# Optimization experiments

Hardware: AMD Instinct MI355X
Metric: run time of the kernel (lower is better)

Reference implementation:

```python
import jax, jax.numpy as jnp
import numpy as np

# ---- static structure for the 28x28 image grid ----
H = 28
V = H * H          # 784 vertices
T = 25             # landscape sample points
K_MAX = 2          # landscape orders kept
M0 = 0.05          # DTM mass parameter

_idx = np.arange(V).reshape(H, H)
_e_h = np.stack([_idx[:, :-1].ravel(), _idx[:, 1:].ravel()], 1)
_e_v = np.stack([_idx[:-1, :].ravel(), _idx[1:, :].ravel()], 1)
EDGES = np.concatenate([_e_h, _e_v], 0).astype(np.int32)   # [E,2], E=1512
E = EDGES.shape[0]

# grid coordinates per lims=[[27,0],[0,27]], normalized to [0,1]
_c0 = np.linspace(1.0, 0.0, H)
_c1 = np.linspace(0.0, 1.0, H)
COORDS = np.stack(np.meshgrid(_c0, _c1, indexing='ij'), -1).reshape(V, 2)
_D2 = ((COORDS[:, None, :] - COORDS[None, :, :]) ** 2).sum(-1)   # [V,V] static
ORDER = jnp.asarray(np.argsort(_D2, 1).astype(np.int32))          # nearest-first per row
D2S = jnp.asarray(np.take_along_axis(_D2, np.argsort(_D2, 1), 1).astype(np.float32))
TSEQ = jnp.asarray(np.linspace(0.0, 0.5, T).astype(np.float32))   # landscape eval grid
EA = jnp.asarray(EDGES[:, 0])
EB = jnp.asarray(EDGES[:, 1])


def _dtm(w):
    """Distance-to-measure filtration on the grid. w: [B,V] pixel masses -> [B,V]."""
    m = w / jnp.clip(jnp.sum(w, 1, keepdims=True), 1e-12)
    ws = m[:, ORDER]                                  # [B,V,V] masses in nearest-first order
    c = jnp.cumsum(ws, -1)
    take = jnp.minimum(ws, jnp.clip(M0 - (c - ws), 0.0, None))  # mass used until m0 reached
    return jnp.sqrt(jnp.sum(take * D2S[None], -1) / M0 + 1e-12)


def _ph0(f):
    """0-dim persistence of sublevel filtration of f on the grid graph (Kruskal/union-find).
    f: [V] -> (births, deaths, valid) each [E]."""
    w = jnp.maximum(f[EA], f[EB])                     # edge filtration values
    o = jnp.argsort(w)
    aa, bb, ww = EA[o], EB[o], w[o]

    def step(carry, e):
        r, bv = carry                                 # r: fully-compressed root per vertex
        ai, bi, wi = e
        ra, rb = r[ai], r[bi]
        diff = ra != rb
        young_a = bv[ra] >= bv[rb]                    # younger comp = larger birth
        young = jnp.where(young_a, ra, rb)
        old = jnp.where(young_a, rb, ra)
        birth = bv[young]
        r = jnp.where(diff & (r == young), old, r)    # merge, keep full compression
        return (r, bv), (birth, wi, diff)

    init = (jnp.arange(V, dtype=jnp.int32), f)
    _, (bs, ds, valid) = jax.lax.scan(step, init, (aa, bb, ww))
    return bs, ds, valid


def _landscape(bs, ds, valid):
    """Persistence landscape lambda_k(t), k<K_MAX, t in TSEQ -> [K_MAX*T] features."""
    tent = jnp.maximum(jnp.minimum(TSEQ[:, None] - bs[None, :], ds[None, :] - TSEQ[:, None]), 0.0)
    tent = tent * valid[None, :]                      # [T,E]
    top = jax.lax.top_k(tent, K_MAX)[0]               # [T,K]
    return top.T.reshape(-1)                          # [K*T] = 50


def setup_inputs() -> dict:
    key = jax.random.key(0)
    k1, k2, k3, k4, k5 = jax.random.split(key, 5)
    return {
        'input': jax.random.uniform(k1, (128, 1, 28, 28), dtype=jnp.float32),
        'w_topo': jax.random.normal(k2, (50, 100), dtype=jnp.float32) * 0.1,
        'b_topo': jax.random.normal(k3, (100,), dtype=jnp.float32) * 0.01,
        'w_fc': jax.random.normal(k4, (100, 10), dtype=jnp.float32) * 0.1,
        'b_fc': jax.random.normal(k5, (10,), dtype=jnp.float32) * 0.01,
    }


def reference(input, w_topo, b_topo, w_fc, b_fc):
    B = input.shape[0]
    x = input.reshape(B, V)
    f = _dtm(x)                                       # [B,V] DTM filtration
    bs, ds, valid = jax.vmap(_ph0)(f)                 # persistence pairs per sample
    feats = jax.vmap(_landscape)(bs, ds, valid.astype(f.dtype))  # [B,50]
    h = jax.nn.relu(feats @ w_topo + b_topo)          # AdTopoLayer linear + ReLU -> [B,100]
    return h @ w_fc + b_fc                            # [B,10]
```

## Files before the change

kernel.cpp:

```cpp
#include <hip/hip_runtime.h>
#include <math.h>

#define HH 28
#define VV 784
#define EE 1512
#define TT 25
#define M0C 0.05


#define DECODE(idx, A, B)                                                  \
  {                                                                        \
    if ((idx) < 756) {                                                     \
      int i_ = (idx) / 27, j_ = (idx) - i_ * 27;                           \
      A = i_ * HH + j_; B = A + 1;                                         \
    } else {                                                               \
      int q_ = (idx) - 756;                                                \
      int i_ = q_ / HH, j_ = q_ - i_ * HH;                                 \
      A = i_ * HH + j_; B = A + HH;                                        \
    }                                                                      \
  }

__global__ __launch_bounds__(512) void k_sortrows(int* __restrict__ ORDER, float* __restrict__ D2S) {
  __shared__ unsigned long long keys[1024];
  const int v = blockIdx.x;
  const int i1 = v / HH, j1 = v % HH;
  const double step = 1.0 / 27.0;
  const double c0v = (i1 == 27) ? 0.0 : 1.0 - (double)i1 * step;
  const double c1v = (j1 == 27) ? 1.0 : (double)j1 * step;
  for (int u = threadIdx.x; u < 1024; u += 512) {
    unsigned long long key = ~0ULL;
    if (u < VV) {
      int i2 = u / HH, j2 = u % HH;
      double c0u = (i2 == 27) ? 0.0 : 1.0 - (double)i2 * step;
      double c1u = (j2 == 27) ? 1.0 : (double)j2 * step;
      double dx = c0v - c0u, dy = c1v - c1u;
      float d2 = (float)(dx * dx + dy * dy);
      key = ((unsigned long long)__float_as_uint(d2) << 32) | (unsigned)u;
    }
    keys[u] = key;
  }
  __syncthreads();
  for (unsigned k = 2; k <= 1024; k <<= 1) {
    for (unsigned j = k >> 1; j; j >>= 1) {
      for (unsigned i = threadIdx.x; i < 1024; i += 512) {
        unsigned l = i ^ j;
        if (l > i) {
          unsigned long long a = keys[i], c = keys[l];
          if ((a > c) == ((i & k) == 0)) { keys[i] = c; keys[l] = a; }
        }
      }
      __syncthreads();
    }
  }
  for (int u = threadIdx.x; u < VV; u += 512) {
    unsigned long long key = keys[u];
    ORDER[v * VV + u] = (int)(key & 0xffffffffu);
    D2S[v * VV + u] = __uint_as_float((unsigned)(key >> 32));
  }
}

__global__ __launch_bounds__(256) void k_norm(const float* __restrict__ x, float* __restrict__ MT) {
  const int b = blockIdx.x;
  const int tid = threadIdx.x;
  double s = 0.0;
  for (int i = tid; i < VV; i += 256) s += (double)x[b * VV + i];
  for (int off = 32; off; off >>= 1) s += __shfl_xor(s, off, 64);
  __shared__ double sred[4];
  __shared__ double Ssh;
  if ((tid & 63) == 0) sred[tid >> 6] = s;
  __syncthreads();
  if (tid == 0) {
    double S = sred[0] + sred[1] + sred[2] + sred[3];
    Ssh = (S > 1e-12) ? S : 1e-12;
  }
  __syncthreads();
  double S = Ssh;
  for (int i = tid; i < VV; i += 256) MT[i * 128 + b] = (float)((double)x[b * VV + i] / S);
}

__global__ __launch_bounds__(128) void k_dtm(const float* __restrict__ MT, const int* __restrict__ ORDER,
                                             const float* __restrict__ D2S, float* __restrict__ F) {
  const int v = blockIdx.x;
  const int tid = threadIdx.x;
  __shared__ int ordS[VV];
  __shared__ float d2sS[VV];
  for (int k = tid; k < VV; k += 128) {
    ordS[k] = ORDER[v * VV + k];
    d2sS[k] = D2S[v * VV + k];
  }
  __syncthreads();
  float P = 0.0f, acc = 0.0f;
  for (int base = 0; base < VV; base += 16) {
    #pragma unroll
    for (int kk = 0; kk < 16; ++kk) {
      int k = base + kk;
      float mass = MT[ordS[k] * 128 + tid];
      float room = (float)M0C - P;
      room = room > 0.0f ? room : 0.0f;
      float take = mass < room ? mass : room;
      acc += take * d2sS[k];
      P += mass;
    }
    if (__all(P >= (float)M0C)) break;
  }
  F[tid * VV + v] = sqrtf(acc / (float)M0C + 1e-12f);
}

__global__ __launch_bounds__(512) void k_main(const float* __restrict__ F,
                                              const float* __restrict__ w_topo, const float* __restrict__ b_topo,
                                              const float* __restrict__ w_fc, const float* __restrict__ b_fc,
                                              float* __restrict__ out) {
  const int b = blockIdx.x;
  const int tid = threadIdx.x;
  __shared__ float fv[VV];
  __shared__ unsigned long long keys[2048];
  __shared__ unsigned long long par64[VV];
  __shared__ unsigned long long pairs[VV];
  __shared__ float feat[2 * TT];
  __shared__ float hbuf[100];
  __shared__ int cntS;
  for (int i = tid; i < VV; i += 512) {
    float f = F[b * VV + i];
    fv[i] = f;
    par64[i] = ((unsigned long long)__float_as_uint(f) << 32) | (unsigned)i;
  }
  __syncthreads();
  for (int e = tid; e < 2048; e += 512) {
    unsigned long long key = 0xFFFFFFFF00000000ULL;
    if (e < EE) {
      int aa, bb;
      DECODE(e, aa, bb);
      float w = fmaxf(fv[aa], fv[bb]);
      unsigned lo = ((e >= 756) ? (1u << 20) : 0u) | ((unsigned)aa << 10) | (unsigned)bb;
      key = ((unsigned long long)__float_as_uint(w) << 32) | lo;
    }
    keys[e] = key;
  }
  __syncthreads();
  for (unsigned k = 2; k <= 2048; k <<= 1) {
    for (unsigned j = k >> 1; j; j >>= 1) {
      for (unsigned i = tid; i < 2048; i += 512) {
        unsigned l = i ^ j;
        if (l > i) {
          unsigned long long a = keys[i], c = keys[l];
          if ((a > c) == ((i & k) == 0)) { keys[i] = c; keys[l] = a; }
        }
      }
      __syncthreads();
    }
  }
  if (tid < 64) {
    const int lane = tid;
    const unsigned long long lbit = 1ULL << lane;
    int cnt = 0;
    unsigned long long K = keys[lane];
    for (int batch = 0; batch < 24; ++batch) {
      unsigned long long Kn = keys[(batch + 1) * 64 + lane];
      unsigned lo = (unsigned)K;
      int aa = (int)((lo >> 10) & 1023), bb = (int)(lo & 1023);
      unsigned wbits = (unsigned)(K >> 32);
      unsigned long long pka = par64[aa], pkb = par64[bb];
      unsigned ra = (unsigned)pka, rb = (unsigned)pkb;
      unsigned fa = (unsigned)(pka >> 32), fb = (unsigned)(pkb >> 32);
      unsigned long long candB = __ballot(ra != rb);
      if (candB) {
        bool rec = false;
        unsigned long long pairv = 0;
        if (__popcll(candB) == 1) {
          if (ra != rb) {
            bool ya = (fa >= fb);
            unsigned young = ya ? ra : rb;
            unsigned oldv = ya ? rb : ra;
            unsigned foldv = ya ? fb : fa;
            unsigned birth = ya ? fa : fb;
            par64[young] = ((unsigned long long)foldv << 32) | oldv;
            pairv = ((unsigned long long)birth << 32) | wbits;
            rec = (wbits > birth);
          }
        } else {
          int merged = 0;
          unsigned young_w = 0;
          unsigned long long oldpk_w = 0;
          #pragma unroll 4
          for (int j = 0; j < 64; ++j) {
            unsigned s_ra = (unsigned)__builtin_amdgcn_readlane((int)ra, j);
            unsigned s_rb = (unsigned)__builtin_amdgcn_readlane((int)rb, j);
            if (s_ra != s_rb) {
              unsigned s_fa = (unsigned)__builtin_amdgcn_readlane((int)fa, j);
              unsigned s_fb = (unsigned)__builtin_amdgcn_readlane((int)fb, j);
              bool ya = (s_fa >= s_fb);
              unsigned young = ya ? s_ra : s_rb;
              unsigned oldv = ya ? s_rb : s_ra;
              unsigned foldv = ya ? s_fb : s_fa;
              unsigned birth = ya ? s_fa : s_fb;
              bool me = (lane == j);
              merged = me ? 1 : merged;
              young_w = me ? young : young_w;
              oldpk_w = me ? (((unsigned long long)foldv << 32) | oldv) : oldpk_w;
              pairv = me ? (((unsigned long long)birth << 32) | wbits) : pairv;
              bool ma = (ra == young);
              ra = ma ? oldv : ra;
              fa = ma ? foldv : fa;
              bool mb2 = (rb == young);
              rb = mb2 ? oldv : rb;
              fb = mb2 ? foldv : fb;
            }
          }
          if (merged) par64[young_w] = oldpk_w;
          rec = merged && ((unsigned)pairv > (unsigned)(pairv >> 32));
        }
        unsigned long long recB = __ballot(rec);
        int rank = __popcll(recB & (lbit - 1ULL));
        if (rec) pairs[cnt + rank] = pairv;
        cnt += (int)__popcll(recB);
        {
          unsigned long long p[13];
          #pragma unroll
          for (int s = 0; s < 12; ++s) p[s] = par64[lane + 64 * s];
          const int i12 = (lane < 16) ? (768 + lane) : lane;
          p[12] = par64[i12];
          for (;;) {
            bool stable = true;
            #pragma unroll
            for (int s = 0; s < 13; ++s) {
              unsigned r = (unsigned)p[s];
              unsigned long long q = par64[r];
              stable &= ((unsigned)q == r);
              p[s] = q;
            }
            if (__all(stable)) break;
          }
          #pragma unroll
          for (int s = 0; s < 12; ++s) par64[lane + 64 * s] = p[s];
          par64[i12] = p[12];
        }
      }
      K = Kn;
    }
    if (lane == 0) cntS = cnt;
  }
  __syncthreads();
  const int cnt = cntS;
  const int wid = tid >> 6, lane = tid & 63;
  for (int t = wid; t < TT; t += 8) {
    double tvd = (t == 24) ? 0.5 : (double)t * (0.5 / 24.0);
    float tv = (float)tvd;
    float m1 = 0.0f, m2 = 0.0f;
    for (int pidx = lane; pidx < cnt; pidx += 64) {
      unsigned long long pr = pairs[pidx];
      float pbv = __uint_as_float((unsigned)(pr >> 32));
      float pdv = __uint_as_float((unsigned)pr);
      float tent = fminf(tv - pbv, pdv - tv);
      tent = fmaxf(tent, 0.0f);
      if (tent > m1) { m2 = m1; m1 = tent; }
      else if (tent > m2) { m2 = tent; }
    }
    #pragma unroll
    for (int off = 32; off; off >>= 1) {
      float o1 = __shfl_xor(m1, off, 64);
      float o2 = __shfl_xor(m2, off, 64);
      float n1 = fmaxf(m1, o1);
      float n2 = fmaxf(fminf(m1, o1), fmaxf(m2, o2));
      m1 = n1; m2 = n2;
    }
    if (lane == 0) { feat[t] = m1; feat[TT + t] = m2; }
  }
  __syncthreads();
  if (tid < 100) {
    double h = (double)b_topo[tid];
    for (int k2 = 0; k2 < 50; ++k2) h += (double)feat[k2] * (double)w_topo[k2 * 100 + tid];
    hbuf[tid] = (h > 0.0) ? (float)h : 0.0f;
  }
  __syncthreads();
  if (tid < 10) {
    double o = (double)b_fc[tid];
    for (int k2 = 0; k2 < 100; ++k2) o += (double)hbuf[k2] * (double)w_fc[k2 * 10 + tid];
    out[b * 10 + tid] = (float)o;
  }
}

extern "C" void kernel_launch(void* const* d_in, const int* in_sizes, int n_in,
                              void* d_out, int out_size, void* d_ws, size_t ws_size,
                              hipStream_t stream) {
  const float* x = (const float*)d_in[0];
  const float* w_topo = (const float*)d_in[1];
  const float* b_topo = (const float*)d_in[2];
  const float* w_fc = (const float*)d_in[3];
  const float* b_fc = (const float*)d_in[4];
  float* outp = (float*)d_out;
  char* ws = (char*)d_ws;
  int* ORDER = (int*)ws;
  float* D2S = (float*)(ws + 2458624);
  float* MT = (float*)(ws + 4917248);
  float* F = (float*)(ws + 5318656);

  hipLaunchKernelGGL(k_sortrows, dim3(VV), dim3(512), 0, stream, ORDER, D2S);
  hipLaunchKernelGGL(k_norm, dim3(128), dim3(256), 0, stream, x, MT);
  hipLaunchKernelGGL(k_dtm, dim3(VV), dim3(128), 0, stream, MT, ORDER, D2S, F);
  hipLaunchKernelGGL(k_main, dim3(128), dim3(512), 0, stream, F, w_topo, b_topo, w_fc, b_fc, outp);
}
```

Measured before the change: 193.7 us.

## Compact candidate lanes before serial merge loop and fuse preprocessing kernels

In the wavefront union-find, edges whose endpoints are in different components are now packed into the low lanes with ds_permute. The serial readlane merge loop then runs only over that candidate count instead of always over 64 lanes, which cuts the serial work in each batch. Separately, the row-sort and normalization kernels are merged into one launch using a block-index split, which removes one kernel launch. The compaction adds five permutes per batch and moves where each merge result is recorded.

```diff
diff --git a/kernel.cpp b/kernel.cpp
--- a/kernel.cpp
+++ b/kernel.cpp
@@ -20,62 +20,66 @@
     }                                                                      \
   }
 
-__global__ __launch_bounds__(512) void k_sortrows(int* __restrict__ ORDER, float* __restrict__ D2S) {
+__global__ __launch_bounds__(512) void k_pre(const float* __restrict__ x,
+                                             int* __restrict__ ORDER, float* __restrict__ D2S,
+                                             float* __restrict__ MT) {
   __shared__ unsigned long long keys[1024];
-  const int v = blockIdx.x;
-  const int i1 = v / HH, j1 = v % HH;
-  const double step = 1.0 / 27.0;
-  const double c0v = (i1 == 27) ? 0.0 : 1.0 - (double)i1 * step;
-  const double c1v = (j1 == 27) ? 1.0 : (double)j1 * step;
-  for (int u = threadIdx.x; u < 1024; u += 512) {
-    unsigned long long key = ~0ULL;
-    if (u < VV) {
-      int i2 = u / HH, j2 = u % HH;
-      double c0u = (i2 == 27) ? 0.0 : 1.0 - (double)i2 * step;
-      double c1u = (j2 == 27) ? 1.0 : (double)j2 * step;
-      double dx = c0v - c0u, dy = c1v - c1u;
-      float d2 = (float)(dx * dx + dy * dy);
-      key = ((unsigned long long)__float_as_uint(d2) << 32) | (unsigned)u;
-    }
-    keys[u] = key;
-  }
-  __syncthreads();
-  for (unsigned k = 2; k <= 1024; k <<= 1) {
-    for (unsigned j = k >> 1; j; j >>= 1) {
-      for (unsigned i = threadIdx.x; i < 1024; i += 512) {
-        unsigned l = i ^ j;
-        if (l > i) {
-          unsigned long long a = keys[i], c = keys[l];
-          if ((a > c) == ((i & k) == 0)) { keys[i] = c; keys[l] = a; }
+  __shared__ double sred[8];
+  __shared__ double Ssh;
+  const int tid = threadIdx.x;
+  if (blockIdx.x < VV) {
+    const int v = blockIdx.x;
+    const int i1 = v / HH, j1 = v % HH;
+    const double step = 1.0 / 27.0;
+    const double c0v = (i1 == 27) ? 0.0 : 1.0 - (double)i1 * step;
+    const double c1v = (j1 == 27) ? 1.0 : (double)j1 * step;
+    for (int u = tid; u < 1024; u += 512) {
+      unsigned long long key = ~0ULL;
+      if (u < VV) {
+        int i2 = u / HH, j2 = u % HH;
+        double c0u = (i2 == 27) ? 0.0 : 1.0 - (double)i2 * step;
+        double c1u = (j2 == 27) ? 1.0 : (double)j2 * step;
+        double dx = c0v - c0u, dy = c1v - c1u;
+        float d2 = (float)(dx * dx + dy * dy);
+        key = ((unsigned long long)__float_as_uint(d2) << 32) | (unsigned)u;
+      }
+      keys[u] = key;
+    }
+    __syncthreads();
+    for (unsigned k = 2; k <= 1024; k <<= 1) {
+      for (unsigned j = k >> 1; j; j >>= 1) {
+        for (unsigned i = tid; i < 1024; i += 512) {
+          unsigned l = i ^ j;
+          if (l > i) {
+            unsigned long long a = keys[i], c = keys[l];
+            if ((a > c) == ((i & k) == 0)) { keys[i] = c; keys[l] = a; }
+          }
         }
+        __syncthreads();
       }
-      __syncthreads();
-    }
-  }
-  for (int u = threadIdx.x; u < VV; u += 512) {
-    unsigned long long key = keys[u];
-    ORDER[v * VV + u] = (int)(key & 0xffffffffu);
-    D2S[v * VV + u] = __uint_as_float((unsigned)(key >> 32));
-  }
-}
-
-__global__ __launch_bounds__(256) void k_norm(const float* __restrict__ x, float* __restrict__ MT) {
-  const int b = blockIdx.x;
-  const int tid = threadIdx.x;
-  double s = 0.0;
-  for (int i = tid; i < VV; i += 256) s += (double)x[b * VV + i];
-  for (int off = 32; off; off >>= 1) s += __shfl_xor(s, off, 64);
-  __shared__ double sred[4];
-  __shared__ double Ssh;
-  if ((tid & 63) == 0) sred[tid >> 6] = s;
-  __syncthreads();
-  if (tid == 0) {
-    double S = sred[0] + sred[1] + sred[2] + sred[3];
-    Ssh = (S > 1e-12) ? S : 1e-12;
-  }
-  __syncthreads();
-  double S = Ssh;
-  for (int i = tid; i < VV; i += 256) MT[i * 128 + b] = (float)((double)x[b * VV + i] / S);
+    }
+    for (int u = tid; u < VV; u += 512) {
+      unsigned long long key = keys[u];
+      ORDER[v * VV + u] = (int)(key & 0xffffffffu);
+      D2S[v * VV + u] = __uint_as_float((unsigned)(key >> 32));
+    }
+  } else {
+    const int b = blockIdx.x - VV;
+    double s = 0.0;
+    for (int i = tid; i < VV; i += 512) s += (double)x[b * VV + i];
+    for (int off = 32; off; off >>= 1) s += __shfl_xor(s, off, 64);
+    if ((tid & 63) == 0) sred[tid >> 6] = s;
+    __syncthreads();
+    if (tid == 0) {
+      double S = 0.0;
+      #pragma unroll
+      for (int wv = 0; wv < 8; ++wv) S += sred[wv];
+      Ssh = (S > 1e-12) ? S : 1e-12;
+    }
+    __syncthreads();
+    double S = Ssh;
+    for (int i = tid; i < VV; i += 512) MT[i * 128 + b] = (float)((double)x[b * VV + i] / S);
+  }
 }
 
 __global__ __launch_bounds__(128) void k_dtm(const float* __restrict__ MT, const int* __restrict__ ORDER,
@@ -162,12 +166,14 @@
       unsigned long long pka = par64[aa], pkb = par64[bb];
       unsigned ra = (unsigned)pka, rb = (unsigned)pkb;
       unsigned fa = (unsigned)(pka >> 32), fb = (unsigned)(pkb >> 32);
-      unsigned long long candB = __ballot(ra != rb);
+      bool isCand = (ra != rb);
+      unsigned long long candB = __ballot(isCand);
       if (candB) {
         bool rec = false;
         unsigned long long pairv = 0;
-        if (__popcll(candB) == 1) {
-          if (ra != rb) {
+        int nc = (int)__popcll(candB);
+        if (nc == 1) {
+          if (isCand) {
             bool ya = (fa >= fb);
             unsigned young = ya ? ra : rb;
             unsigned oldv = ya ? rb : ra;
@@ -178,33 +184,40 @@
             rec = (wbits > birth);
           }
         } else {
+          int rankC = (int)__popcll(candB & (lbit - 1ULL));
+          int rankN = nc + (int)__popcll((~candB) & (lbit - 1ULL));
+          int dst = (isCand ? rankC : rankN) << 2;
+          unsigned cra = (unsigned)__builtin_amdgcn_ds_permute(dst, (int)ra);
+          unsigned crb = (unsigned)__builtin_amdgcn_ds_permute(dst, (int)rb);
+          unsigned cfa = (unsigned)__builtin_amdgcn_ds_permute(dst, (int)fa);
+          unsigned cfb = (unsigned)__builtin_amdgcn_ds_permute(dst, (int)fb);
+          unsigned cw = (unsigned)__builtin_amdgcn_ds_permute(dst, (int)wbits);
           int merged = 0;
           unsigned young_w = 0;
           unsigned long long oldpk_w = 0;
-          #pragma unroll 4
-          for (int j = 0; j < 64; ++j) {
-            unsigned s_ra = (unsigned)__builtin_amdgcn_readlane((int)ra, j);
-            unsigned s_rb = (unsigned)__builtin_amdgcn_readlane((int)rb, j);
-            if (s_ra != s_rb) {
-              unsigned s_fa = (unsigned)__builtin_amdgcn_readlane((int)fa, j);
-              unsigned s_fb = (unsigned)__builtin_amdgcn_readlane((int)fb, j);
-              bool ya = (s_fa >= s_fb);
-              unsigned young = ya ? s_ra : s_rb;
-              unsigned oldv = ya ? s_rb : s_ra;
-              unsigned foldv = ya ? s_fb : s_fa;
-              unsigned birth = ya ? s_fa : s_fb;
-              bool me = (lane == j);
-              merged = me ? 1 : merged;
-              young_w = me ? young : young_w;
-              oldpk_w = me ? (((unsigned long long)foldv << 32) | oldv) : oldpk_w;
-              pairv = me ? (((unsigned long long)birth << 32) | wbits) : pairv;
-              bool ma = (ra == young);
-              ra = ma ? oldv : ra;
-              fa = ma ? foldv : fa;
-              bool mb2 = (rb == young);
-              rb = mb2 ? oldv : rb;
-              fb = mb2 ? foldv : fb;
-            }
+          for (int j = 0; j < nc; ++j) {
+            unsigned s_ra = (unsigned)__builtin_amdgcn_readlane((int)cra, j);
+            unsigned s_rb = (unsigned)__builtin_amdgcn_readlane((int)crb, j);
+            unsigned s_fa = (unsigned)__builtin_amdgcn_readlane((int)cfa, j);
+            unsigned s_fb = (unsigned)__builtin_amdgcn_readlane((int)cfb, j);
+            bool sdf = (s_ra != s_rb);
+            bool ya = (s_fa >= s_fb);
+            unsigned young = ya ? s_ra : s_rb;
+            unsigned oldv = ya ? s_rb : s_ra;
+            unsigned foldv = ya ? s_fb : s_fa;
+            unsigned birth = ya ? s_fa : s_fb;
+            unsigned young_eff = sdf ? young : 0xFFFFFFFFu;
+            bool me = (lane == j) & sdf;
+            merged = me ? 1 : merged;
+            young_w = me ? young : young_w;
+            oldpk_w = me ? (((unsigned long long)foldv << 32) | oldv) : oldpk_w;
+            pairv = me ? (((unsigned long long)birth << 32) | cw) : pairv;
+            bool ma = (cra == young_eff);
+            cra = ma ? oldv : cra;
+            cfa = ma ? foldv : cfa;
+            bool mb2 = (crb == young_eff);
+            crb = mb2 ? oldv : crb;
+            cfb = mb2 ? foldv : cfb;
           }
           if (merged) par64[young_w] = oldpk_w;
           rec = merged && ((unsigned)pairv > (unsigned)(pairv >> 32));
@@ -294,8 +307,7 @@
   float* MT = (float*)(ws + 4917248);
   float* F = (float*)(ws + 5318656);
 
-  hipLaunchKernelGGL(k_sortrows, dim3(VV), dim3(512), 0, stream, ORDER, D2S);
-  hipLaunchKernelGGL(k_norm, dim3(128), dim3(256), 0, stream, x, MT);
+  hipLaunchKernelGGL(k_pre, dim3(VV + 128), dim3(512), 0, stream, x, ORDER, D2S, MT);
   hipLaunchKernelGGL(k_dtm, dim3(VV), dim3(128), 0, stream, MT, ORDER, D2S, F);
   hipLaunchKernelGGL(k_main, dim3(128), dim3(512), 0, stream, F, w_topo, b_topo, w_fc, b_fc, outp);
 }
```

After: 251.4 us. 29.8% more time.
